# Optimization experiments

Measured on AMD Instinct MI355X. Metric: run time of the kernel, lower is better.

The kernel has to match this reference:

```python
import jax, jax.numpy as jnp
import numpy as np

B, S, H = 4, 4096, 1024
NUM_LEVELS, DECAY = 3, 0.8
D0, D1 = 512, 204  # int(1024*0.5), int(512*0.5*0.8)


def _xavier(key, shape):
    fan_in, fan_out = shape
    return jax.random.normal(key, shape, dtype=jnp.float32) * np.sqrt(2.0 / (fan_in + fan_out))


def setup_inputs() -> dict:
    key = jax.random.key(0)
    ks = jax.random.split(key, 8)
    return {
        "keys": jax.random.normal(ks[0], (B, S, H), dtype=jnp.float32),
        "values": jax.random.normal(ks[1], (B, S, H), dtype=jnp.float32),
        "importance": jax.random.uniform(ks[2], (B, S), dtype=jnp.float32),
        # encoder layers (stored as [in, out]; torch Linear applies x @ W.T + b)
        "We0": _xavier(ks[3], (H, D0)), "be0": jnp.zeros((D0,), jnp.float32),
        "We1": _xavier(ks[4], (D0, D1)), "be1": jnp.zeros((D1,), jnp.float32),
        # decoder layers
        "Wd0": _xavier(ks[5], (D0, H)), "bd0": jnp.zeros((H,), jnp.float32),
        "Wd1": _xavier(ks[6], (D1, D0)), "bd1": jnp.zeros((D0,), jnp.float32),
    }


def _level_sizes(n):
    sizes, remaining = [], n
    for i in range(NUM_LEVELS):
        if i == NUM_LEVELS - 1:
            sizes.append(remaining)
        else:
            sz = int(remaining * (1 - DECAY) * DECAY ** i)
            sizes.append(sz)
            remaining -= sz
    return sizes


def reference(keys, values, importance, We0, be0, We1, be1, Wd0, bd0, Wd1, bd1):
    n = B * S
    fk = keys.reshape(n, H)
    fv = values.reshape(n, H)
    sorted_idx = jnp.argsort(-importance.reshape(-1))  # descending importance
    sizes = _level_sizes(n)

    def chain(x, level):
        # encode 0..level-1 with ReLU, then decode level-1..0 with ReLU
        if level >= 1:
            x = jax.nn.relu(x @ We0 + be0)
        if level >= 2:
            x = jax.nn.relu(x @ We1 + be1)
            x = jax.nn.relu(x @ Wd1 + bd1)
        if level >= 1:
            x = jax.nn.relu(x @ Wd0 + bd0)
        return x

    ck = jnp.zeros_like(fk)
    cv = jnp.zeros_like(fv)
    start = 0
    for level, size in enumerate(sizes):
        if size <= 0:
            continue
        idx = jax.lax.dynamic_slice(sorted_idx, (start,), (size,))
        ck = ck.at[idx].set(chain(fk[idx], level))
        cv = cv.at[idx].set(chain(fv[idx], level))
        start += size
    return ck.reshape(B, S, H), cv.reshape(B, S, H)
```

## Files before the change

kernel.cpp:

```cpp
#include <hip/hip_runtime.h>

typedef __attribute__((ext_vector_type(8))) short short8;
typedef __attribute__((ext_vector_type(4))) float f32x4;

#define N_TOK   16384
#define HDIM    1024
#define OUT_OFF 16777216
#define M1ROWS  26216
#define M2ROWS  22022
#define L2ROW0  4194

__device__ __forceinline__ unsigned short f2bf(float f) {
  unsigned int u = __float_as_uint(f);
  u += 0x7FFFu + ((u >> 16) & 1u);
  return (unsigned short)(u >> 16);
}

__device__ __forceinline__ void rowmap(int r, int& is_v, int& rank) {
  if (r < 2097)       { is_v = 0; rank = 3276 + r; }
  else if (r < 4194)  { is_v = 1; rank = 1179 + r; }
  else if (r < 15205) { is_v = 0; rank = 1179 + r; }
  else                { is_v = 1; rank = r - 9832; }
}

__global__ __launch_bounds__(256) void rank_count(const float* __restrict__ imp,
                                                  int* __restrict__ counts) {
  __shared__ float sj[2048];
  const int i = blockIdx.x * 256 + threadIdx.x;
  const int jbase = blockIdx.y * 2048;
  const float vi = imp[i];
  for (int s = threadIdx.x; s < 2048; s += 256) sj[s] = imp[jbase + s];
  __syncthreads();
  int cnt = 0;
  #pragma unroll 8
  for (int s = 0; s < 2048; ++s) {
    float vj = sj[s];
    bool gt = vj > vi;
    bool eq = (vj == vi) && ((jbase + s) < i);
    cnt += (gt || eq) ? 1 : 0;
  }
  atomicAdd(&counts[i], cnt);
}

__global__ __launch_bounds__(256) void scatter_order(const int* __restrict__ counts,
                                                     int* __restrict__ order) {
  int i = blockIdx.x * 256 + threadIdx.x;
  order[counts[i]] = i;
}

__global__ __launch_bounds__(256) void wconv(unsigned short* __restrict__ dst,
                                             const float* __restrict__ src,
                                             int Nd, int Kd, int Nsrc, int Ksrc) {
  int idx = blockIdx.x * 256 + threadIdx.x;
  if (idx >= Nd * Kd) return;
  int n = idx / Kd, k = idx % Kd;
  float v = (n < Nsrc && k < Ksrc) ? src[k * Nsrc + n] : 0.f;
  dst[idx] = f2bf(v);
}

__global__ __launch_bounds__(256) void gather_rows(unsigned short* __restrict__ X,
                                                   const float* __restrict__ keys,
                                                   const float* __restrict__ values,
                                                   const int* __restrict__ order) {
  int r = blockIdx.x;
  int is_v, rank; rowmap(r, is_v, rank);
  int token = order[rank];
  const float* src = (is_v ? values : keys) + (size_t)token * HDIM;
  int c = threadIdx.x * 4;
  float4 f = *reinterpret_cast<const float4*>(src + c);
  ushort4 h;
  h.x = f2bf(f.x); h.y = f2bf(f.y); h.z = f2bf(f.z); h.w = f2bf(f.w);
  *reinterpret_cast<ushort4*>(X + (size_t)r * HDIM + c) = h;
}

__global__ __launch_bounds__(256) void copy_level0(float* __restrict__ out,
                                                   const float* __restrict__ keys,
                                                   const float* __restrict__ values,
                                                   const int* __restrict__ order) {
  int b = blockIdx.x;
  int is_v = b & 1, rank = b >> 1;
  int token = order[rank];
  const float* src = (is_v ? values : keys) + (size_t)token * HDIM;
  float* dst = out + (is_v ? OUT_OFF : 0) + (size_t)token * HDIM;
  int c = threadIdx.x * 4;
  *reinterpret_cast<float4*>(dst + c) = *reinterpret_cast<const float4*>(src + c);
}

#define GLDS16(g, l) __builtin_amdgcn_global_load_lds( \
    (const __attribute__((address_space(1))) void*)(g), \
    (__attribute__((address_space(3))) void*)(l), 16, 0, 0)

template<int MODE>
__global__ __launch_bounds__(256) void gemm_bias_relu(
    const unsigned short* __restrict__ A, int M, int K,
    const unsigned short* __restrict__ Bt, int N,
    const float* __restrict__ bias, int Nbias,
    unsigned short* __restrict__ Cbf, int ldc,
    float* __restrict__ outf, const int* __restrict__ order,
    int NP, int NC) {
  __shared__ __align__(16) unsigned short As[3][128 * 32];
  __shared__ __align__(16) unsigned short Bs[3][128 * 32];
  const int bid = blockIdx.x;
  const int r8 = bid & 7;
  const int rest = bid >> 3;
  const int c8 = rest % NC;
  const int q8 = rest / NC;
  const int p8 = q8 * 8 + r8;
  if (p8 >= NP) return;
  const int row0 = p8 * 128, col0 = c8 * 128;

  const int tid = threadIdx.x;
  const int wave = tid >> 6, lane = tid & 63;
  const int lrow = lane >> 2;
  const int lk = (((lane & 3) ^ ((lane >> 3) & 3)) << 3);
  const int wr = (wave >> 1) * 64, wc = (wave & 1) * 64;

  const int s0 = wave * 2, s1 = wave * 2 + 1;
  int ar0 = row0 + s0 * 16 + lrow; if (ar0 >= M) ar0 = 0;
  int ar1 = row0 + s1 * 16 + lrow; if (ar1 >= M) ar1 = 0;
  int br0 = col0 + s0 * 16 + lrow; if (br0 >= N) br0 = 0;
  int br1 = col0 + s1 * 16 + lrow; if (br1 >= N) br1 = 0;
  const unsigned short* ap0 = A + (size_t)ar0 * K + lk;
  const unsigned short* ap1 = A + (size_t)ar1 * K + lk;
  const unsigned short* bp0 = Bt + (size_t)br0 * K + lk;
  const unsigned short* bp1 = Bt + (size_t)br1 * K + lk;

  f32x4 acc[4][4] = {};
  const int fr = lane & 15;
  const int qoff = (((lane >> 4) ^ ((fr >> 1) & 3)) << 3);

  const int nt = K >> 5;
  GLDS16(ap0, As[0] + s0 * 512);
  GLDS16(ap1, As[0] + s1 * 512);
  GLDS16(bp0, Bs[0] + s0 * 512);
  GLDS16(bp1, Bs[0] + s1 * 512);
  GLDS16(ap0 + 32, As[1] + s0 * 512);
  GLDS16(ap1 + 32, As[1] + s1 * 512);
  GLDS16(bp0 + 32, Bs[1] + s0 * 512);
  GLDS16(bp1 + 32, Bs[1] + s1 * 512);

  int cur = 0;
  for (int t = 0; t < nt; ++t) {
    if (t + 1 < nt) asm volatile("s_waitcnt vmcnt(4)" ::: "memory");
    else            asm volatile("s_waitcnt vmcnt(0)" ::: "memory");
    __builtin_amdgcn_s_barrier();
    __builtin_amdgcn_sched_barrier(0);
    const unsigned short* as = As[cur];
    const unsigned short* bs = Bs[cur];
    short8 af[4], bfv[4];
    #pragma unroll
    for (int m = 0; m < 4; ++m)
      af[m] = *reinterpret_cast<const short8*>(as + (wr + m * 16 + fr) * 32 + qoff);
    #pragma unroll
    for (int n = 0; n < 4; ++n)
      bfv[n] = *reinterpret_cast<const short8*>(bs + (wc + n * 16 + fr) * 32 + qoff);
    if (t + 2 < nt) {
      const int k2 = (t + 2) << 5;
      int nb = cur + 2; if (nb >= 3) nb -= 3;
      GLDS16(ap0 + k2, As[nb] + s0 * 512);
      GLDS16(ap1 + k2, As[nb] + s1 * 512);
      GLDS16(bp0 + k2, Bs[nb] + s0 * 512);
      GLDS16(bp1 + k2, Bs[nb] + s1 * 512);
    }
    #pragma unroll
    for (int m = 0; m < 4; ++m)
      #pragma unroll
      for (int n = 0; n < 4; ++n)
        acc[m][n] = __builtin_amdgcn_mfma_f32_16x16x32_bf16(af[m], bfv[n], acc[m][n], 0, 0, 0);
    cur = (cur == 2) ? 0 : cur + 1;
  }

  const int orow = (lane >> 4) * 4;
  const int ocol = lane & 15;
  #pragma unroll
  for (int m = 0; m < 4; ++m) {
    #pragma unroll
    for (int n = 0; n < 4; ++n) {
      #pragma unroll
      for (int j = 0; j < 4; ++j) {
        int r = row0 + wr + m * 16 + orow + j;
        int c = col0 + wc + n * 16 + ocol;
        if (r < M && c < N) {
          float v = acc[m][n][j] + (c < Nbias ? bias[c] : 0.f);
          v = fmaxf(v, 0.f);
          if (MODE == 0) {
            Cbf[(size_t)r * ldc + c] = f2bf(v);
          } else {
            int iv, rk; rowmap(r, iv, rk);
            int token = order[rk];
            outf[(size_t)(iv ? OUT_OFF : 0) + (size_t)token * HDIM + c] = v;
          }
        }
      }
    }
  }
}

static inline int swz_grid(int NP, int NC) { return 8 * NC * ((NP + 7) / 8); }

extern "C" void kernel_launch(void* const* d_in, const int* in_sizes, int n_in,
                              void* d_out, int out_size, void* d_ws, size_t ws_size,
                              hipStream_t stream) {
  const float* keys   = (const float*)d_in[0];
  const float* values = (const float*)d_in[1];
  const float* imp    = (const float*)d_in[2];
  const float* We0    = (const float*)d_in[3];
  const float* be0    = (const float*)d_in[4];
  const float* We1    = (const float*)d_in[5];
  const float* be1    = (const float*)d_in[6];
  const float* Wd0    = (const float*)d_in[7];
  const float* bd0    = (const float*)d_in[8];
  const float* Wd1    = (const float*)d_in[9];
  const float* bd1    = (const float*)d_in[10];

  char* ws = (char*)d_ws;
  int* counts           = (int*)(ws);
  int* order            = (int*)(ws + 65536);
  unsigned short* We0T  = (unsigned short*)(ws + 131072);
  unsigned short* We1T  = (unsigned short*)(ws + 1179648);
  unsigned short* Wd1T  = (unsigned short*)(ws + 1409024);
  unsigned short* Wd0T  = (unsigned short*)(ws + 1638400);
  unsigned short* Y     = (unsigned short*)(ws + 2686976);
  unsigned short* Z     = (unsigned short*)(ws + 29532160);
  unsigned short* X = (unsigned short*)d_out;
  float* outf = (float*)d_out;

  hipMemsetAsync(counts, 0, 65536, stream);
  rank_count<<<dim3(64, 8), 256, 0, stream>>>(imp, counts);
  scatter_order<<<64, 256, 0, stream>>>(counts, order);

  wconv<<<2048, 256, 0, stream>>>(We0T, We0, 512, 1024, 512, 1024);
  wconv<<<448,  256, 0, stream>>>(We1T, We1, 224, 512, 204, 512);
  wconv<<<448,  256, 0, stream>>>(Wd1T, Wd1, 512, 224, 512, 204);
  wconv<<<2048, 256, 0, stream>>>(Wd0T, Wd0, 1024, 512, 1024, 512);

  gather_rows<<<M1ROWS, 256, 0, stream>>>(X, keys, values, order);

  gemm_bias_relu<0><<<swz_grid(205, 4), 256, 0, stream>>>(
      X, M1ROWS, 1024, We0T, 512, be0, 512, Y, 512, nullptr, nullptr, 205, 4);

  copy_level0<<<6552, 256, 0, stream>>>(outf, keys, values, order);

  gemm_bias_relu<0><<<swz_grid(173, 2), 256, 0, stream>>>(
      Y + (size_t)L2ROW0 * 512, M2ROWS, 512, We1T, 224, be1, 204, Z, 224,
      nullptr, nullptr, 173, 2);

  gemm_bias_relu<0><<<swz_grid(173, 4), 256, 0, stream>>>(
      Z, M2ROWS, 224, Wd1T, 512, bd1, 512, Y + (size_t)L2ROW0 * 512, 512,
      nullptr, nullptr, 173, 4);

  gemm_bias_relu<1><<<swz_grid(205, 8), 256, 0, stream>>>(
      Y, M1ROWS, 512, Wd0T, 1024, bd0, 1024, nullptr, 0, outf, order, 205, 8);
}
```

Baseline: 304.2 us.

## Enlarge GEMM tile to 256x128 with 8 waves and unified LDS buffer

Doubles the row dimension of each GEMM block tile from 128 to 256 and runs 8 waves (512 threads) per block. A and B now share one LDS buffer per stage, with each wave issuing three global-to-LDS loads per k-step instead of four. The wait count drops to match. The goal is better reuse of the B tile and fewer blocks, at the cost of more LDS per block (72KB), fewer resident blocks and more tail waste from partial row tiles.

```diff
diff --git a/kernel.cpp b/kernel.cpp
--- a/kernel.cpp
+++ b/kernel.cpp
@@ -91,15 +91,14 @@
     (__attribute__((address_space(3))) void*)(l), 16, 0, 0)
 
 template<int MODE>
-__global__ __launch_bounds__(256) void gemm_bias_relu(
+__global__ __launch_bounds__(512) void gemm_bias_relu(
     const unsigned short* __restrict__ A, int M, int K,
     const unsigned short* __restrict__ Bt, int N,
     const float* __restrict__ bias, int Nbias,
     unsigned short* __restrict__ Cbf, int ldc,
     float* __restrict__ outf, const int* __restrict__ order,
     int NP, int NC) {
-  __shared__ __align__(16) unsigned short As[3][128 * 32];
-  __shared__ __align__(16) unsigned short Bs[3][128 * 32];
+  __shared__ __align__(16) unsigned short S[3][12288];
   const int bid = blockIdx.x;
   const int r8 = bid & 7;
   const int rest = bid >> 3;
@@ -107,7 +106,7 @@
   const int q8 = rest / NC;
   const int p8 = q8 * 8 + r8;
   if (p8 >= NP) return;
-  const int row0 = p8 * 128, col0 = c8 * 128;
+  const int row0 = p8 * 256, col0 = c8 * 128;
 
   const int tid = threadIdx.x;
   const int wave = tid >> 6, lane = tid & 63;
@@ -115,38 +114,37 @@
   const int lk = (((lane & 3) ^ ((lane >> 3) & 3)) << 3);
   const int wr = (wave >> 1) * 64, wc = (wave & 1) * 64;
 
-  const int s0 = wave * 2, s1 = wave * 2 + 1;
-  int ar0 = row0 + s0 * 16 + lrow; if (ar0 >= M) ar0 = 0;
-  int ar1 = row0 + s1 * 16 + lrow; if (ar1 >= M) ar1 = 0;
-  int br0 = col0 + s0 * 16 + lrow; if (br0 >= N) br0 = 0;
-  int br1 = col0 + s1 * 16 + lrow; if (br1 >= N) br1 = 0;
-  const unsigned short* ap0 = A + (size_t)ar0 * K + lk;
-  const unsigned short* ap1 = A + (size_t)ar1 * K + lk;
-  const unsigned short* bp0 = Bt + (size_t)br0 * K + lk;
-  const unsigned short* bp1 = Bt + (size_t)br1 * K + lk;
+  const unsigned short* gp[3];
+  int ldso[3];
+  #pragma unroll
+  for (int j = 0; j < 3; ++j) {
+    const int g = wave * 3 + j;
+    const bool isA = g < 16;
+    int rr = isA ? (row0 + g * 16 + lrow) : (col0 + (g - 16) * 16 + lrow);
+    const int lim = isA ? M : N;
+    if (rr >= lim) rr = 0;
+    gp[j] = (isA ? A : Bt) + (size_t)rr * K + lk;
+    ldso[j] = g * 512;
+  }
 
   f32x4 acc[4][4] = {};
   const int fr = lane & 15;
   const int qoff = (((lane >> 4) ^ ((fr >> 1) & 3)) << 3);
 
   const int nt = K >> 5;
-  GLDS16(ap0, As[0] + s0 * 512);
-  GLDS16(ap1, As[0] + s1 * 512);
-  GLDS16(bp0, Bs[0] + s0 * 512);
-  GLDS16(bp1, Bs[0] + s1 * 512);
-  GLDS16(ap0 + 32, As[1] + s0 * 512);
-  GLDS16(ap1 + 32, As[1] + s1 * 512);
-  GLDS16(bp0 + 32, Bs[1] + s0 * 512);
-  GLDS16(bp1 + 32, Bs[1] + s1 * 512);
+  #pragma unroll
+  for (int j = 0; j < 3; ++j) GLDS16(gp[j], S[0] + ldso[j]);
+  #pragma unroll
+  for (int j = 0; j < 3; ++j) GLDS16(gp[j] + 32, S[1] + ldso[j]);
 
   int cur = 0;
   for (int t = 0; t < nt; ++t) {
-    if (t + 1 < nt) asm volatile("s_waitcnt vmcnt(4)" ::: "memory");
+    if (t + 1 < nt) asm volatile("s_waitcnt vmcnt(3)" ::: "memory");
     else            asm volatile("s_waitcnt vmcnt(0)" ::: "memory");
     __builtin_amdgcn_s_barrier();
     __builtin_amdgcn_sched_barrier(0);
-    const unsigned short* as = As[cur];
-    const unsigned short* bs = Bs[cur];
+    const unsigned short* as = S[cur];
+    const unsigned short* bs = S[cur] + 8192;
     short8 af[4], bfv[4];
     #pragma unroll
     for (int m = 0; m < 4; ++m)
@@ -157,10 +155,8 @@
     if (t + 2 < nt) {
       const int k2 = (t + 2) << 5;
       int nb = cur + 2; if (nb >= 3) nb -= 3;
-      GLDS16(ap0 + k2, As[nb] + s0 * 512);
-      GLDS16(ap1 + k2, As[nb] + s1 * 512);
-      GLDS16(bp0 + k2, Bs[nb] + s0 * 512);
-      GLDS16(bp1 + k2, Bs[nb] + s1 * 512);
+      #pragma unroll
+      for (int j = 0; j < 3; ++j) GLDS16(gp[j] + k2, S[nb] + ldso[j]);
     }
     #pragma unroll
     for (int m = 0; m < 4; ++m)
@@ -236,19 +232,19 @@
 
   gather_rows<<<M1ROWS, 256, 0, stream>>>(X, keys, values, order);
 
-  gemm_bias_relu<0><<<swz_grid(205, 4), 256, 0, stream>>>(
-      X, M1ROWS, 1024, We0T, 512, be0, 512, Y, 512, nullptr, nullptr, 205, 4);
+  gemm_bias_relu<0><<<swz_grid(103, 4), 512, 0, stream>>>(
+      X, M1ROWS, 1024, We0T, 512, be0, 512, Y, 512, nullptr, nullptr, 103, 4);
 
   copy_level0<<<6552, 256, 0, stream>>>(outf, keys, values, order);
 
-  gemm_bias_relu<0><<<swz_grid(173, 2), 256, 0, stream>>>(
+  gemm_bias_relu<0><<<swz_grid(87, 2), 512, 0, stream>>>(
       Y + (size_t)L2ROW0 * 512, M2ROWS, 512, We1T, 224, be1, 204, Z, 224,
-      nullptr, nullptr, 173, 2);
-
-  gemm_bias_relu<0><<<swz_grid(173, 4), 256, 0, stream>>>(
+      nullptr, nullptr, 87, 2);
+
+  gemm_bias_relu<0><<<swz_grid(87, 4), 512, 0, stream>>>(
       Z, M2ROWS, 224, Wd1T, 512, bd1, 512, Y + (size_t)L2ROW0 * 512, 512,
-      nullptr, nullptr, 173, 4);
-
-  gemm_bias_relu<1><<<swz_grid(205, 8), 256, 0, stream>>>(
-      Y, M1ROWS, 512, Wd0T, 1024, bd0, 1024, nullptr, 0, outf, order, 205, 8);
-}
+      nullptr, nullptr, 87, 4);
+
+  gemm_bias_relu<1><<<swz_grid(103, 8), 512, 0, stream>>>(
+      Y, M1ROWS, 512, Wd0T, 1024, bd0, 1024, nullptr, 0, outf, order, 103, 8);
+}
```

Measured after the change: 274.4 us. 1.11x faster.
